# Optimization experiments

Hardware: AMD Instinct MI355X
Metric: run time of the kernel (lower is better)

Reference implementation:

```python
import jax, jax.numpy as jnp
import numpy as np

V, D, K = 400000, 300, 10

def setup_inputs() -> dict:
    key = jax.random.key(0)
    k1, k2 = jax.random.split(key)
    word2vec = jax.random.normal(k1, (V, D), dtype=jnp.float32)  # embedding table
    w = jax.random.normal(k2, (D,), dtype=jnp.float32)           # query vector
    return {"word2vec": word2vec, "w": w, "k": K}

def reference(word2vec, w, k):
    # cosine similarity: (word2vec @ w) / (||rows|| * ||w||), matching torch eps placement
    dots = word2vec @ w                                          # [V]
    row_norms = jnp.sqrt(jnp.sum(word2vec * word2vec, axis=1) + 1e-9)  # [V]
    q_norm = jnp.sqrt(jnp.sum(w * w))
    cos = dots / (row_norms * q_norm)                            # [V]
    vals, topk = jax.lax.top_k(cos, k)                           # top-k neighbors
    return vals, topk
```

## Files before the change

kernel.cpp:

```cpp
#include <hip/hip_runtime.h>

#define D    300
#define NF4  75
#define K    10
#define WPB  4
#define GPB  16
#define NBLOCKS 2048
#define NGROUPS (NBLOCKS * GPB)

#define P2_BLOCKS  256
#define P2_THREADS 1024
#define P2_CPT     2
#define NCAND      (P2_BLOCKS * K)
#define F_CPT      3

typedef float f32x4 __attribute__((ext_vector_type(4)));

__device__ __forceinline__ f32x4 ntload(const f32x4* p) {
    return __builtin_nontemporal_load(p);
}

__device__ __forceinline__ float d4(f32x4 a, f32x4 b) {
    return a[0]*b[0] + a[1]*b[1] + a[2]*b[2] + a[3]*b[3];
}

#define RED16(x) { x += __shfl_xor(x, 8, 64); x += __shfl_xor(x, 4, 64); \
                   x += __shfl_xor(x, 2, 64); x += __shfl_xor(x, 1, 64); }

__global__ __launch_bounds__(256) void cos_all(
    const float* __restrict__ emb, const float* __restrict__ wvec,
    float* __restrict__ score, int V, int s)
{
    const int tid  = threadIdx.x;
    const int lane = tid & 63;
    const int wid  = tid >> 6;
    const int l16  = lane & 15;
    const int rg   = lane >> 4;
    const bool tl  = (l16 < NF4 - 64);

    const f32x4* w4p = (const f32x4*)wvec;
    f32x4 w0 = w4p[l16];
    f32x4 w1 = w4p[l16 + 16];
    f32x4 w2 = w4p[l16 + 32];
    f32x4 w3 = w4p[l16 + 48];
    f32x4 w4t = 0.f;
    if (tl) w4t = w4p[l16 + 64];

    float qsq = d4(w0,w0)+d4(w1,w1)+d4(w2,w2)+d4(w3,w3)+d4(w4t,w4t);
    RED16(qsq);
    const float qn = sqrtf(qsq);

    const int g0 = (blockIdx.x * WPB + wid) * 4 + rg;
    const size_t stepF4 = (size_t)s * NF4;

    const f32x4* p = (const f32x4*)emb + (size_t)g0 * NF4 + l16;

#define BODY(a0,a1,a2,a3,a4, ROW)                            \
    {   float da = d4(a0,w0) + d4(a1,w1);                    \
        float db = d4(a2,w2) + d4(a3,w3) + d4(a4,w4t);       \
        float sa = d4(a0,a0) + d4(a1,a1);                    \
        float sb = d4(a2,a2) + d4(a3,a3) + d4(a4,a4);        \
        float dot = da + db;                                 \
        float sq  = sa + sb;                                 \
        RED16(dot); RED16(sq);                               \
        float c = dot / (sqrtf(sq + 1e-9f) * qn);            \
        if (l16 == 0) score[ROW] = c; }

    int r = g0;
    while (r < V) {
        {
            f32x4 a0 = p[0];
            f32x4 a1 = p[16];
            f32x4 a2 = p[32];
            f32x4 a3 = p[48];
            f32x4 a4 = 0.f;
            if (tl) a4 = p[64];
            BODY(a0,a1,a2,a3,a4, r)
            r += s; p += stepF4;
        }
        if (r < V) {
            f32x4 a0 = ntload(p);
            f32x4 a1 = ntload(p + 16);
            f32x4 a2 = ntload(p + 32);
            f32x4 a3 = ntload(p + 48);
            f32x4 a4 = 0.f;
            if (tl) a4 = ntload(p + 64);
            BODY(a0,a1,a2,a3,a4, r)
            r += s; p += stepF4;
        }
    }
#undef BODY
}

__global__ __launch_bounds__(P2_THREADS) void block_topk(
    const float* __restrict__ score, int V,
    float* __restrict__ cand_v, int* __restrict__ cand_i)
{
    __shared__ float rv[16];
    __shared__ int   rp[16];
    __shared__ int   s_bp;

    const int tid  = threadIdx.x;
    const int lane = tid & 63;
    const int wid  = tid >> 6;
    const int per  = (V + P2_BLOCKS - 1) / P2_BLOCKS;
    const int base = blockIdx.x * per;

    float v[P2_CPT];
    #pragma unroll
    for (int t = 0; t < P2_CPT; ++t) {
        int i = tid + t * P2_THREADS;
        v[t] = (i < per && base + i < V) ? score[base + i] : -3e38f;
    }

    for (int p = 0; p < K; ++p) {
        float bestv = -3e38f; int bestpos = 0x7fffffff;
        #pragma unroll
        for (int t = 0; t < P2_CPT; ++t) {
            if (v[t] > bestv) { bestv = v[t]; bestpos = tid + t * P2_THREADS; }
        }
        #pragma unroll
        for (int m = 32; m >= 1; m >>= 1) {
            float ov = __shfl_xor(bestv, m, 64);
            int   op = __shfl_xor(bestpos, m, 64);
            if (ov > bestv || (ov == bestv && op < bestpos)) { bestv = ov; bestpos = op; }
        }
        if (lane == 0) { rv[wid] = bestv; rp[wid] = bestpos; }
        __syncthreads();
        if (tid == 0) {
            float bv = rv[0]; int bp = rp[0];
            for (int i = 1; i < 16; ++i)
                if (rv[i] > bv || (rv[i] == bv && rp[i] < bp)) { bv = rv[i]; bp = rp[i]; }
            cand_v[blockIdx.x*K + p] = bv;
            cand_i[blockIdx.x*K + p] = base + bp;
            s_bp = bp;
        }
        __syncthreads();
        const int wbp = s_bp;
        #pragma unroll
        for (int t = 0; t < P2_CPT; ++t) {
            if (tid + t * P2_THREADS == wbp) v[t] = -3e38f;
        }
        __syncthreads();
    }
}

__global__ __launch_bounds__(P2_THREADS) void final_topk(
    const float* __restrict__ cand_v, const int* __restrict__ cand_i,
    float* __restrict__ out)
{
    __shared__ float rv[16];
    __shared__ int   rp[16];
    __shared__ int   s_bp;

    const int tid  = threadIdx.x;
    const int lane = tid & 63;
    const int wid  = tid >> 6;

    float v[F_CPT];
    #pragma unroll
    for (int t = 0; t < F_CPT; ++t) {
        int i = tid + t * P2_THREADS;
        v[t] = (i < NCAND) ? cand_v[i] : -3e38f;
    }

    for (int p = 0; p < K; ++p) {
        float bestv = -3e38f; int bestpos = 0x7fffffff;
        #pragma unroll
        for (int t = 0; t < F_CPT; ++t) {
            if (v[t] > bestv) { bestv = v[t]; bestpos = tid + t * P2_THREADS; }
        }
        #pragma unroll
        for (int m = 32; m >= 1; m >>= 1) {
            float ov = __shfl_xor(bestv, m, 64);
            int   op = __shfl_xor(bestpos, m, 64);
            if (ov > bestv || (ov == bestv && op < bestpos)) { bestv = ov; bestpos = op; }
        }
        if (lane == 0) { rv[wid] = bestv; rp[wid] = bestpos; }
        __syncthreads();
        if (tid == 0) {
            float bv = rv[0]; int bp = rp[0];
            for (int i = 1; i < 16; ++i)
                if (rv[i] > bv || (rv[i] == bv && rp[i] < bp)) { bv = rv[i]; bp = rp[i]; }
            out[p]     = bv;
            out[K + p] = (float)cand_i[bp];
            s_bp = bp;
        }
        __syncthreads();
        const int wbp = s_bp;
        #pragma unroll
        for (int t = 0; t < F_CPT; ++t) {
            if (tid + t * P2_THREADS == wbp) v[t] = -3e38f;
        }
        __syncthreads();
    }
}

extern "C" void kernel_launch(void* const* d_in, const int* in_sizes, int n_in,
                              void* d_out, int out_size, void* d_ws, size_t ws_size,
                              hipStream_t stream) {
    const float* emb  = (const float*)d_in[0];
    const float* wvec = (const float*)d_in[1];
    const int V = in_sizes[0] / D;

    float* score  = (float*)d_ws;
    float* cand_v = score + V;
    int*   cand_i = (int*)(cand_v + NCAND);

    cos_all<<<NBLOCKS, 256, 0, stream>>>(emb, wvec, score, V, NGROUPS);
    block_topk<<<P2_BLOCKS, P2_THREADS, 0, stream>>>(score, V, cand_v, cand_i);
    final_topk<<<1, P2_THREADS, 0, stream>>>(cand_v, cand_i, (float*)d_out);
}
```

Measured before the change: 119.9 us.

## Fuse per-group top-k selection into cosine kernel and drop block_topk pass

Each 16-lane row group keeps a register-resident sorted top-10 list while streaming rows, then the block merges its 16 group lists in shared memory and writes 10 candidates per block. This removes the score array write/read and the separate block_topk kernel launch. In exchange, the final kernel must now reduce 20480 candidates with 20 values per thread, its 10 passes each run with more work per pass, and the insertion sort adds divergent register work in the streaming loop. Every lane of a group computes the same cosine value, so the lanes agree on whether to insert.

After: 121.0 us. About the same (+0.8%).

```diff
diff --git a/kernel.cpp b/kernel.cpp
--- a/kernel.cpp
+++ b/kernel.cpp
@@ -8,11 +8,9 @@
 #define NBLOCKS 2048
 #define NGROUPS (NBLOCKS * GPB)
 
-#define P2_BLOCKS  256
-#define P2_THREADS 1024
-#define P2_CPT     2
-#define NCAND      (P2_BLOCKS * K)
-#define F_CPT      3
+#define NCAND      (NBLOCKS * K)
+#define F_THREADS  1024
+#define F_CPT      20
 
 typedef float f32x4 __attribute__((ext_vector_type(4)));
 
@@ -27,9 +25,10 @@
 #define RED16(x) { x += __shfl_xor(x, 8, 64); x += __shfl_xor(x, 4, 64); \
                    x += __shfl_xor(x, 2, 64); x += __shfl_xor(x, 1, 64); }
 
-__global__ __launch_bounds__(256) void cos_all(
+__global__ __launch_bounds__(256) void cos_topk(
     const float* __restrict__ emb, const float* __restrict__ wvec,
-    float* __restrict__ score, int V, int s)
+    float* __restrict__ cand_v, int* __restrict__ cand_i,
+    int V, int s)
 {
     const int tid  = threadIdx.x;
     const int lane = tid & 63;
@@ -50,21 +49,34 @@
     RED16(qsq);
     const float qn = sqrtf(qsq);
 
+    float tv[K]; int ti[K];
+    #pragma unroll
+    for (int j = 0; j < K; ++j) { tv[j] = -3e38f; ti[j] = 0; }
+
     const int g0 = (blockIdx.x * WPB + wid) * 4 + rg;
     const size_t stepF4 = (size_t)s * NF4;
-
     const f32x4* p = (const f32x4*)emb + (size_t)g0 * NF4 + l16;
 
-#define BODY(a0,a1,a2,a3,a4, ROW)                            \
-    {   float da = d4(a0,w0) + d4(a1,w1);                    \
-        float db = d4(a2,w2) + d4(a3,w3) + d4(a4,w4t);       \
-        float sa = d4(a0,a0) + d4(a1,a1);                    \
-        float sb = d4(a2,a2) + d4(a3,a3) + d4(a4,a4);        \
-        float dot = da + db;                                 \
-        float sq  = sa + sb;                                 \
-        RED16(dot); RED16(sq);                               \
-        float c = dot / (sqrtf(sq + 1e-9f) * qn);            \
-        if (l16 == 0) score[ROW] = c; }
+#define BODY(a0,a1,a2,a3,a4, ROW)                                \
+    {   float da = d4(a0,w0) + d4(a1,w1);                        \
+        float db = d4(a2,w2) + d4(a3,w3) + d4(a4,w4t);           \
+        float sa = d4(a0,a0) + d4(a1,a1);                        \
+        float sb = d4(a2,a2) + d4(a3,a3) + d4(a4,a4);            \
+        float dot = da + db;                                     \
+        float sq  = sa + sb;                                     \
+        RED16(dot); RED16(sq);                                   \
+        float c = dot / (sqrtf(sq + 1e-9f) * qn);                \
+        if (c > tv[K-1]) {                                       \
+            tv[K-1] = c; ti[K-1] = (ROW);                        \
+            _Pragma("unroll")                                    \
+            for (int j = K-1; j > 0; --j) {                      \
+                if (tv[j] > tv[j-1]) {                           \
+                    float t = tv[j]; tv[j] = tv[j-1]; tv[j-1] = t;\
+                    int   u = ti[j]; ti[j] = ti[j-1]; ti[j-1] = u;\
+                }                                                \
+            }                                                    \
+        }                                                        \
+    }
 
     int r = g0;
     while (r < V) {
@@ -90,62 +102,41 @@
         }
     }
 #undef BODY
-}
 
-__global__ __launch_bounds__(P2_THREADS) void block_topk(
-    const float* __restrict__ score, int V,
-    float* __restrict__ cand_v, int* __restrict__ cand_i)
-{
-    __shared__ float rv[16];
-    __shared__ int   rp[16];
-    __shared__ int   s_bp;
-
-    const int tid  = threadIdx.x;
-    const int lane = tid & 63;
-    const int wid  = tid >> 6;
-    const int per  = (V + P2_BLOCKS - 1) / P2_BLOCKS;
-    const int base = blockIdx.x * per;
-
-    float v[P2_CPT];
-    #pragma unroll
-    for (int t = 0; t < P2_CPT; ++t) {
-        int i = tid + t * P2_THREADS;
-        v[t] = (i < per && base + i < V) ? score[base + i] : -3e38f;
+    __shared__ float sv[GPB * K];
+    __shared__ int   si[GPB * K];
+    if (l16 == 0) {
+        const int gidx = wid * 4 + rg;
+        #pragma unroll
+        for (int j = 0; j < K; ++j) { sv[gidx*K + j] = tv[j]; si[gidx*K + j] = ti[j]; }
     }
-
-    for (int p = 0; p < K; ++p) {
-        float bestv = -3e38f; int bestpos = 0x7fffffff;
+    __syncthreads();
+    if (tid == 0) {
+        float bv[K]; int bi[K];
         #pragma unroll
-        for (int t = 0; t < P2_CPT; ++t) {
-            if (v[t] > bestv) { bestv = v[t]; bestpos = tid + t * P2_THREADS; }
+        for (int j = 0; j < K; ++j) { bv[j] = -3e38f; bi[j] = 0; }
+        for (int t = 0; t < GPB * K; ++t) {
+            float c = sv[t]; int rr = si[t];
+            if (c > bv[K-1]) {
+                bv[K-1] = c; bi[K-1] = rr;
+                #pragma unroll
+                for (int j = K-1; j > 0; --j) {
+                    if (bv[j] > bv[j-1]) {
+                        float t2 = bv[j]; bv[j] = bv[j-1]; bv[j-1] = t2;
+                        int   u2 = bi[j]; bi[j] = bi[j-1]; bi[j-1] = u2;
+                    }
+                }
+            }
         }
         #pragma unroll
-        for (int m = 32; m >= 1; m >>= 1) {
-            float ov = __shfl_xor(bestv, m, 64);
-            int   op = __shfl_xor(bestpos, m, 64);
-            if (ov > bestv || (ov == bestv && op < bestpos)) { bestv = ov; bestpos = op; }
+        for (int j = 0; j < K; ++j) {
+            cand_v[blockIdx.x*K + j] = bv[j];
+            cand_i[blockIdx.x*K + j] = bi[j];
         }
-        if (lane == 0) { rv[wid] = bestv; rp[wid] = bestpos; }
-        __syncthreads();
-        if (tid == 0) {
-            float bv = rv[0]; int bp = rp[0];
-            for (int i = 1; i < 16; ++i)
-                if (rv[i] > bv || (rv[i] == bv && rp[i] < bp)) { bv = rv[i]; bp = rp[i]; }
-            cand_v[blockIdx.x*K + p] = bv;
-            cand_i[blockIdx.x*K + p] = base + bp;
-            s_bp = bp;
-        }
-        __syncthreads();
-        const int wbp = s_bp;
-        #pragma unroll
-        for (int t = 0; t < P2_CPT; ++t) {
-            if (tid + t * P2_THREADS == wbp) v[t] = -3e38f;
-        }
-        __syncthreads();
     }
 }
 
-__global__ __launch_bounds__(P2_THREADS) void final_topk(
+__global__ __launch_bounds__(F_THREADS) void final_topk(
     const float* __restrict__ cand_v, const int* __restrict__ cand_i,
     float* __restrict__ out)
 {
@@ -159,16 +150,13 @@
 
     float v[F_CPT];
     #pragma unroll
-    for (int t = 0; t < F_CPT; ++t) {
-        int i = tid + t * P2_THREADS;
-        v[t] = (i < NCAND) ? cand_v[i] : -3e38f;
-    }
+    for (int t = 0; t < F_CPT; ++t) v[t] = cand_v[tid + t * F_THREADS];
 
     for (int p = 0; p < K; ++p) {
         float bestv = -3e38f; int bestpos = 0x7fffffff;
         #pragma unroll
         for (int t = 0; t < F_CPT; ++t) {
-            if (v[t] > bestv) { bestv = v[t]; bestpos = tid + t * P2_THREADS; }
+            if (v[t] > bestv) { bestv = v[t]; bestpos = tid + t * F_THREADS; }
         }
         #pragma unroll
         for (int m = 32; m >= 1; m >>= 1) {
@@ -190,7 +178,7 @@
         const int wbp = s_bp;
         #pragma unroll
         for (int t = 0; t < F_CPT; ++t) {
-            if (tid + t * P2_THREADS == wbp) v[t] = -3e38f;
+            if (tid + t * F_THREADS == wbp) v[t] = -3e38f;
         }
         __syncthreads();
     }
@@ -203,11 +191,9 @@
     const float* wvec = (const float*)d_in[1];
     const int V = in_sizes[0] / D;
 
-    float* score  = (float*)d_ws;
-    float* cand_v = score + V;
+    float* cand_v = (float*)d_ws;
     int*   cand_i = (int*)(cand_v + NCAND);
 
-    cos_all<<<NBLOCKS, 256, 0, stream>>>(emb, wvec, score, V, NGROUPS);
-    block_topk<<<P2_BLOCKS, P2_THREADS, 0, stream>>>(score, V, cand_v, cand_i);
-    final_topk<<<1, P2_THREADS, 0, stream>>>(cand_v, cand_i, (float*)d_out);
+    cos_topk<<<NBLOCKS, 256, 0, stream>>>(emb, wvec, cand_v, cand_i, V, NGROUPS);
+    final_topk<<<1, F_THREADS, 0, stream>>>(cand_v, cand_i, (float*)d_out);
 }
```
